# Performance work log

Hardware: AMD Instinct MI355X
Metric: run time of the kernel (lower is better)

## Reference

```python
import jax, jax.numpy as jnp
import numpy as np

B, L, DM, H = 2, 2048, 512, 8
D = DM // H
FACTOR = 5
NUM_K = int(FACTOR * np.ceil(np.log(L)))  # 40
NUM_Q = NUM_K  # q_len == k_len here
EPS = 1e-5


def setup_inputs() -> dict:
    key = jax.random.key(0)
    ks = jax.random.split(key, 12)
    s = DM ** -0.5
    return {
        "q": jax.random.normal(ks[0], (B, L, DM), jnp.float32),
        "k": jax.random.normal(ks[1], (B, L, DM), jnp.float32),
        "v": jax.random.normal(ks[2], (B, L, DM), jnp.float32),
        "Wq": jax.random.normal(ks[3], (DM, DM), jnp.float32) * s,
        "bq": jnp.zeros((DM,), jnp.float32),
        "Wk": jax.random.normal(ks[4], (DM, DM), jnp.float32) * s,
        "bk": jnp.zeros((DM,), jnp.float32),
        "Wv": jax.random.normal(ks[5], (DM, DM), jnp.float32) * s,
        "bv": jnp.zeros((DM,), jnp.float32),
        "gamma": jnp.ones((DM,), jnp.float32),
        "beta": jnp.zeros((DM,), jnp.float32),
        "random_index": jax.random.randint(ks[6], (L, NUM_K), 0, L, jnp.int32),
    }


def _heads(x):
    # [B, L, DM] -> [B, H, L, D]
    return x.reshape(B, L, H, D).transpose(0, 2, 1, 3)


def reference(q, k, v, Wq, bq, Wk, bk, Wv, bv, gamma, beta, random_index):
    qp = _heads(q @ Wq + bq)
    kp = _heads(k @ Wk + bk)
    vp = _heads(v @ Wv + bv)

    # ProbSparse: sample NUM_K keys per query position (shared over batch/head)
    k_samp = kp[:, :, random_index, :]                      # [B,H,L,NUM_K,D]
    pre = jnp.einsum('bhid,bhijd->bhij', qp, k_samp)        # [B,H,L,NUM_K]
    measure = pre.max(-1) - pre.sum(-1) / L                 # sparsity measure [B,H,L]
    _, q_idx = jax.lax.top_k(measure, NUM_Q)                # [B,H,NUM_Q]

    q_sel = jnp.take_along_axis(qp, q_idx[..., None], axis=2)   # [B,H,NUM_Q,D]
    attn = jnp.einsum('bhid,bhjd->bhij', q_sel, kp) * D ** -0.5 # [B,H,NUM_Q,L]
    attn = jax.nn.softmax(attn, axis=-1)                    # dropout = identity (eval)
    out_sel = jnp.einsum('bhij,bhjd->bhid', attn, vp)       # [B,H,NUM_Q,D]

    # use_mask=False path: context is the mean of v over keys
    v_mean = vp.mean(axis=2)                                # [B,H,D]
    context = jnp.broadcast_to(v_mean[:, :, None, :], (B, H, L, D))
    bi = jnp.arange(B)[:, None, None]
    hi = jnp.arange(H)[None, :, None]
    out = context.at[bi, hi, q_idx].set(out_sel)            # scatter selected rows

    out = out.transpose(0, 2, 1, 3).reshape(B, L, DM)
    y = out + q
    mu = y.mean(-1, keepdims=True)
    var = y.var(-1, keepdims=True)
    yn = (y - mu) / jnp.sqrt(var + EPS) * gamma + beta
    return (yn, attn)
```

## Files before the change

### kernel.cpp

```cpp
#include <hip/hip_runtime.h>
#include <math.h>

#define BB 2
#define LL 2048
#define DMM 512
#define HH 8
#define DD 64
#define NUMK 40
#define NUMQ 40
#define LNEPS 1e-5f
#define LSEG 128
#define NLS 16

typedef unsigned short ushort_t;
typedef __attribute__((ext_vector_type(8))) short bf16x8;
typedef __attribute__((ext_vector_type(4))) float f32x4;

__device__ inline ushort_t f2bf(float x) {
    union { float f; unsigned int u; } v; v.f = x;
    unsigned int r = v.u + 0x7fffu + ((v.u >> 16) & 1u);
    return (ushort_t)(r >> 16);
}
__device__ inline float bf2f(ushort_t h) {
    union { unsigned int u; float f; } v; v.u = ((unsigned int)h) << 16;
    return v.f;
}

__global__ __launch_bounds__(256) void convert_x_kernel(
    const float* __restrict__ q, const float* __restrict__ k, const float* __restrict__ v,
    ushort_t* __restrict__ Xh, ushort_t* __restrict__ Xl) {
    const size_t plane = (size_t)BB * LL * DMM;
    const float* X = (blockIdx.y == 0) ? q : (blockIdx.y == 1) ? k : v;
    ushort_t* xh = Xh + plane * blockIdx.y;
    ushort_t* xl = Xl + plane * blockIdx.y;
    const size_t base = ((size_t)blockIdx.x * 256 + threadIdx.x) * 8;
    float4 a = *(const float4*)(X + base);
    float4 b = *(const float4*)(X + base + 4);
    float xs[8] = {a.x, a.y, a.z, a.w, b.x, b.y, b.z, b.w};
    unsigned int hp[4], lp[4];
#pragma unroll
    for (int j = 0; j < 4; ++j) {
        ushort_t h0 = f2bf(xs[2 * j]),     h1 = f2bf(xs[2 * j + 1]);
        ushort_t l0 = f2bf(xs[2 * j] - bf2f(h0));
        ushort_t l1 = f2bf(xs[2 * j + 1] - bf2f(h1));
        hp[j] = (unsigned int)h0 | ((unsigned int)h1 << 16);
        lp[j] = (unsigned int)l0 | ((unsigned int)l1 << 16);
    }
    *(uint4*)(xh + base) = make_uint4(hp[0], hp[1], hp[2], hp[3]);
    *(uint4*)(xl + base) = make_uint4(lp[0], lp[1], lp[2], lp[3]);
}

__global__ __launch_bounds__(256) void convert_w_kernel(
    const float* __restrict__ Wq, const float* __restrict__ Wk, const float* __restrict__ Wv,
    ushort_t* __restrict__ Wht, ushort_t* __restrict__ Wlt) {
    __shared__ float tile[64][65];
    const size_t plane = (size_t)DMM * DMM;
    const float* W = (blockIdx.z == 0) ? Wq : (blockIdx.z == 1) ? Wk : Wv;
    ushort_t* wht = Wht + plane * blockIdx.z;
    ushort_t* wlt = Wlt + plane * blockIdx.z;
    const int n0 = blockIdx.x * 64, k0 = blockIdx.y * 64;
    const int t = threadIdx.x;
    const int d = t & 63, g = t >> 6;
    for (int rr = g; rr < 64; rr += 4)
        tile[rr][d] = W[(size_t)(k0 + rr) * DMM + n0 + d];
    __syncthreads();
    for (int cc = g; cc < 64; cc += 4) {
        float x = tile[d][cc];
        ushort_t hi = f2bf(x);
        ushort_t lo = f2bf(x - bf2f(hi));
        wht[(size_t)(n0 + cc) * DMM + k0 + d] = hi;
        wlt[(size_t)(n0 + cc) * DMM + k0 + d] = lo;
    }
}

__device__ inline void stage_one(const ushort_t* __restrict__ g, ushort_t* lbuf,
                                 int r0, int lane, int k0) {
    const int r = r0 + (lane >> 3);
    const int c = (lane & 7) ^ (r & 7);
    const ushort_t* gp = g + (size_t)r * DMM + k0 + c * 8;
    __builtin_amdgcn_global_load_lds(
        (const __attribute__((address_space(1))) unsigned int*)gp,
        (__attribute__((address_space(3))) unsigned int*)(lbuf + (size_t)r0 * 64),
        16, 0, 0);
}
__device__ inline bf16x8 frag_ld(const ushort_t* buf, int row, int c) {
    const int idx = row * 8 + (c ^ (row & 7));
    return *(const bf16x8*)(buf + idx * 8);
}

__global__ __launch_bounds__(256, 2) void proj_mfma_kernel(
    const ushort_t* __restrict__ Xh, const ushort_t* __restrict__ Xl,
    const ushort_t* __restrict__ Wht, const ushort_t* __restrict__ Wlt,
    const float* __restrict__ bq, const float* __restrict__ bk, const float* __restrict__ bv,
    float* __restrict__ Oq, float* __restrict__ Ok, float* __restrict__ Ov) {
    const int orig = blockIdx.x;
    const int c = (orig & 7) * 48 + (orig >> 3);
    const int jb = c & 3, mb = (c >> 2) & 31, z = c >> 7;

    const size_t xplane = (size_t)BB * LL * DMM;
    const size_t wplane = (size_t)DMM * DMM;
    const ushort_t* ah_g = Xh + xplane * z;
    const ushort_t* al_g = Xl + xplane * z;
    const ushort_t* bh_g = Wht + wplane * z;
    const ushort_t* bl_g = Wlt + wplane * z;
    const float* bias = (z == 0) ? bq : (z == 1) ? bk : bv;
    float* Out = (z == 0) ? Oq : (z == 1) ? Ok : Ov;

    __shared__ __align__(16) ushort_t bufAh[128 * 64];
    __shared__ __align__(16) ushort_t bufAl[128 * 64];
    __shared__ __align__(16) ushort_t bufBh[128 * 64];
    __shared__ __align__(16) ushort_t bufBl[128 * 64];

    const int t = threadIdx.x;
    const int lane = t & 63, w = t >> 6;
    const int wm = (w & 1) * 64, wn = (w >> 1) * 64;
    const int m0 = mb * 128, j0 = jb * 128;

    const ushort_t* A_h = ah_g + (size_t)m0 * DMM;
    const ushort_t* A_l = al_g + (size_t)m0 * DMM;
    const ushort_t* B_h = bh_g + (size_t)j0 * DMM;
    const ushort_t* B_l = bl_g + (size_t)j0 * DMM;

    f32x4 acc[4][4];
#pragma unroll
    for (int i = 0; i < 4; ++i)
#pragma unroll
        for (int j = 0; j < 4; ++j) acc[i][j] = (f32x4){0.f, 0.f, 0.f, 0.f};

    for (int ch = 0; ch < 8; ++ch) {
        const int k0 = ch * 64;
#pragma unroll
        for (int i = 0; i < 4; ++i) {
            const int r0 = (w * 4 + i) * 8;
            stage_one(A_h, bufAh, r0, lane, k0);
            stage_one(A_l, bufAl, r0, lane, k0);
            stage_one(B_h, bufBh, r0, lane, k0);
            stage_one(B_l, bufBl, r0, lane, k0);
        }
        __syncthreads();
#pragma unroll
        for (int ks = 0; ks < 2; ++ks) {
            const int cc = ks * 4 + (lane >> 4);
            bf16x8 fah[4], fal[4];
#pragma unroll
            for (int tm = 0; tm < 4; ++tm) {
                const int row = wm + tm * 16 + (lane & 15);
                fah[tm] = frag_ld(bufAh, row, cc);
                fal[tm] = frag_ld(bufAl, row, cc);
            }
#pragma unroll
            for (int tn = 0; tn < 4; ++tn) {
                const int rowb = wn + tn * 16 + (lane & 15);
                const bf16x8 fbh = frag_ld(bufBh, rowb, cc);
                const bf16x8 fbl = frag_ld(bufBl, rowb, cc);
#pragma unroll
                for (int tm = 0; tm < 4; ++tm) {
                    acc[tm][tn] = __builtin_amdgcn_mfma_f32_16x16x32_bf16(fah[tm], fbh, acc[tm][tn], 0, 0, 0);
                    acc[tm][tn] = __builtin_amdgcn_mfma_f32_16x16x32_bf16(fal[tm], fbh, acc[tm][tn], 0, 0, 0);
                    acc[tm][tn] = __builtin_amdgcn_mfma_f32_16x16x32_bf16(fah[tm], fbl, acc[tm][tn], 0, 0, 0);
                }
            }
        }
        __syncthreads();
    }

#pragma unroll
    for (int tn = 0; tn < 4; ++tn) {
        const int gn = j0 + wn + tn * 16 + (lane & 15);
        const float bvv = bias[gn];
        const int h = gn >> 6, d = gn & 63;
#pragma unroll
        for (int tm = 0; tm < 4; ++tm) {
#pragma unroll
            for (int reg = 0; reg < 4; ++reg) {
                const int gm = m0 + wm + tm * 16 + (lane >> 4) * 4 + reg;
                const int b = gm >> 11, l = gm & (LL - 1);
                Out[(((size_t)(b * HH + h)) * LL + l) * DD + d] = acc[tm][tn][reg] + bvv;
            }
        }
    }
}

__global__ __launch_bounds__(256) void measure_kernel(const float* __restrict__ qp2,
                                                      const float* __restrict__ kp2,
                                                      const int* __restrict__ rnd,
                                                      float* __restrict__ measure) {
    const int t = threadIdx.x;
    const int lane = t & 63;
    const int wv = t >> 6;
    const int g = lane >> 4;
    const int dq = (lane & 15) * 4;
    const int bh = blockIdx.x;
    const int i = blockIdx.y * 16 + wv * 4 + g;
    const float4 qv = *(const float4*)(qp2 + ((size_t)bh * LL + i) * DD + dq);
    const float* kbase = kp2 + (size_t)bh * LL * DD;
    const int* rp = rnd + i * NUMK;
    float mx = -INFINITY, sm = 0.f;
#pragma unroll 8
    for (int j = 0; j < NUMK; ++j) {
        const int row = rp[j];
        const float4 kv = *(const float4*)(kbase + (size_t)row * DD + dq);
        float p = kv.x * qv.x;
        p = fmaf(kv.y, qv.y, p); p = fmaf(kv.z, qv.z, p); p = fmaf(kv.w, qv.w, p);
        p += __shfl_xor(p, 1, 64);
        p += __shfl_xor(p, 2, 64);
        p += __shfl_xor(p, 4, 64);
        p += __shfl_xor(p, 8, 64);
        mx = fmaxf(mx, p);
        sm += p;
    }
    if ((lane & 15) == 0) measure[(size_t)bh * LL + i] = mx - sm * (1.0f / LL);
}

__global__ __launch_bounds__(256) void topk_kernel(const float* __restrict__ measure,
                                                   int* __restrict__ q_idx,
                                                   int* __restrict__ sel_pos) {
    __shared__ unsigned int keys[LL];
    __shared__ int hist[256];
    __shared__ unsigned int prefix_sh;
    __shared__ int need_sh;
    __shared__ unsigned int cval[256];
    __shared__ int cidx[256];
    __shared__ int cnt;
    const int t = threadIdx.x;
    const int bh = blockIdx.x;
    for (int i = t; i < LL; i += 256) {
        const float f = measure[(size_t)bh * LL + i];
        unsigned int u = __float_as_uint(f);
        keys[i] = (u & 0x80000000u) ? ~u : (u | 0x80000000u);
        sel_pos[(size_t)bh * LL + i] = -1;
    }
    if (t == 0) { prefix_sh = 0u; need_sh = NUMQ; cnt = 0; }
    __syncthreads();

    for (int round = 0; round < 4; ++round) {
        const int shift = 24 - round * 8;
        hist[t] = 0;
        __syncthreads();
        const unsigned int pref = prefix_sh;
        const unsigned int mask = (round == 0) ? 0u : (0xFFFFFFFFu << (shift + 8));
        for (int i = t; i < LL; i += 256) {
            const unsigned int key = keys[i];
            if ((key & mask) == pref)
                atomicAdd(&hist[(key >> shift) & 0xFF], 1);
        }
        __syncthreads();
        if (t == 0) {
            const int need = need_sh;
            int acc = 0;
            int v = 255;
            for (; v > 0; --v) {
                if (acc + hist[v] >= need) break;
                acc += hist[v];
            }
            need_sh = need - acc;
            prefix_sh = pref | ((unsigned int)v << shift);
        }
        __syncthreads();
    }
    const unsigned int K40 = prefix_sh;

    for (int i = t; i < LL; i += 256) {
        if (keys[i] >= K40) {
            int p = atomicAdd(&cnt, 1);
            if (p < 256) { cval[p] = keys[i]; cidx[p] = i; }
        }
    }
    __syncthreads();
    int M = cnt; if (M > 256) M = 256;
    for (int i = t; i < M; i += 256) {
        const unsigned int ki = cval[i];
        const int ii = cidx[i];
        int r = 0;
        for (int j = 0; j < M; ++j) {
            const unsigned int kj = cval[j];
            r += (kj > ki || (kj == ki && cidx[j] < ii)) ? 1 : 0;
        }
        if (r < NUMQ) {
            q_idx[bh * NUMQ + r] = ii;
            sel_pos[(size_t)bh * LL + ii] = r;
        }
    }
}

__global__ __launch_bounds__(256) void attn_part_kernel(
    const float* __restrict__ qp2, const float* __restrict__ kp2,
    const float* __restrict__ vp2, const int* __restrict__ q_idx,
    float* __restrict__ attn_out, float* __restrict__ part_m,
    float* __restrict__ part_s, float* __restrict__ part_pv) {
    __shared__ __align__(16) float Qs[NUMQ][68];
    __shared__ __align__(16) float Ks[LSEG * 64];
    __shared__ __align__(16) float Vs[LSEG * 64];
    __shared__ __align__(16) float Ss[NUMQ][136];
    const int t = threadIdx.x;
    const int lane = t & 63, w = t >> 6;
    const int bh = blockIdx.x;
    const int ls = blockIdx.y;
    const int l0 = ls * LSEG;

    for (int idx = t; idx < NUMQ * 16; idx += 256) {
        const int r = idx >> 4, c4 = idx & 15;
        const int qi = q_idx[bh * NUMQ + r];
        float4 v = *(const float4*)(qp2 + ((size_t)bh * LL + qi) * DD + c4 * 4);
        Qs[r][c4 * 4 + 0] = v.x * 0.125f;
        Qs[r][c4 * 4 + 1] = v.y * 0.125f;
        Qs[r][c4 * 4 + 2] = v.z * 0.125f;
        Qs[r][c4 * 4 + 3] = v.w * 0.125f;
    }

    const float* kseg = kp2 + ((size_t)bh * LL + l0) * DD;
    const float* vseg = vp2 + ((size_t)bh * LL + l0) * DD;
#pragma unroll
    for (int i = 0; i < 8; ++i) {
        const int r0 = (w * 8 + i) * 4;
        const int r = r0 + (lane >> 4);
        const int cg = (lane & 15) ^ (r & 15);
        __builtin_amdgcn_global_load_lds(
            (const __attribute__((address_space(1))) unsigned int*)(kseg + (size_t)r * DD + cg * 4),
            (__attribute__((address_space(3))) unsigned int*)(Ks + r0 * 64), 16, 0, 0);
        __builtin_amdgcn_global_load_lds(
            (const __attribute__((address_space(1))) unsigned int*)(vseg + (size_t)r * DD + cg * 4),
            (__attribute__((address_space(3))) unsigned int*)(Vs + r0 * 64), 16, 0, 0);
    }
    __syncthreads();

    const int qt = t >> 5;
    const int jt = t & 31;
    float acc[5][4];
#pragma unroll
    for (int i = 0; i < 5; ++i)
#pragma unroll
        for (int jj = 0; jj < 4; ++jj) acc[i][jj] = 0.f;

    for (int c4 = 0; c4 < 16; ++c4) {
        float4 q4[5];
#pragma unroll
        for (int i = 0; i < 5; ++i)
            q4[i] = *(const float4*)&Qs[qt + 8 * i][c4 * 4];
#pragma unroll
        for (int jj = 0; jj < 4; ++jj) {
            const int r = jt + 32 * jj;
            const float4 k4 = *(const float4*)&Ks[r * 64 + ((c4 ^ (r & 15)) * 4)];
#pragma unroll
            for (int i = 0; i < 5; ++i) {
                acc[i][jj] = fmaf(q4[i].x, k4.x, acc[i][jj]);
                acc[i][jj] = fmaf(q4[i].y, k4.y, acc[i][jj]);
                acc[i][jj] = fmaf(q4[i].z, k4.z, acc[i][jj]);
                acc[i][jj] = fmaf(q4[i].w, k4.w, acc[i][jj]);
            }
        }
    }

#pragma unroll
    for (int i = 0; i < 5; ++i) {
        const int r = qt + 8 * i;
        float m = fmaxf(fmaxf(acc[i][0], acc[i][1]), fmaxf(acc[i][2], acc[i][3]));
        m = fmaxf(m, __shfl_xor(m, 16, 64));
        m = fmaxf(m, __shfl_xor(m, 8, 64));
        m = fmaxf(m, __shfl_xor(m, 4, 64));
        m = fmaxf(m, __shfl_xor(m, 2, 64));
        m = fmaxf(m, __shfl_xor(m, 1, 64));
        float p0 = __expf(acc[i][0] - m), p1 = __expf(acc[i][1] - m);
        float p2 = __expf(acc[i][2] - m), p3 = __expf(acc[i][3] - m);
        Ss[r][jt]      = p0;
        Ss[r][jt + 32] = p1;
        Ss[r][jt + 64] = p2;
        Ss[r][jt + 96] = p3;
        float s = p0 + p1 + p2 + p3;
        s += __shfl_xor(s, 16, 64);
        s += __shfl_xor(s, 8, 64);
        s += __shfl_xor(s, 4, 64);
        s += __shfl_xor(s, 2, 64);
        s += __shfl_xor(s, 1, 64);
        if (jt == 0) {
            const int row = bh * NUMQ + r;
            part_m[row * NLS + ls] = m;
            part_s[row * NLS + ls] = s;
        }
    }
    __syncthreads();

    for (int idx = t; idx < NUMQ * 32; idx += 256) {
        const int r = idx >> 5, c4 = idx & 31;
        const float4 v = *(const float4*)&Ss[r][c4 * 4];
        *(float4*)(attn_out + (size_t)(bh * NUMQ + r) * LL + l0 + c4 * 4) = v;
    }

    const int dt = t & 31;
    float o[5][2];
#pragma unroll
    for (int i = 0; i < 5; ++i) { o[i][0] = 0.f; o[i][1] = 0.f; }
#pragma unroll 4
    for (int j = 0; j < LSEG; ++j) {
        const int pg = (dt >> 1) ^ (j & 15);
        const float* vr = &Vs[j * 64 + pg * 4 + (dt & 1) * 2];
        const float v0 = vr[0], v1 = vr[1];
#pragma unroll
        for (int i = 0; i < 5; ++i) {
            const float p = Ss[qt + 8 * i][j];
            o[i][0] = fmaf(p, v0, o[i][0]);
            o[i][1] = fmaf(p, v1, o[i][1]);
        }
    }
#pragma unroll
    for (int i = 0; i < 5; ++i) {
        const int row = bh * NUMQ + qt + 8 * i;
        float* pp = part_pv + ((size_t)row * NLS + ls) * DD + dt * 2;
        pp[0] = o[i][0];
        pp[1] = o[i][1];
    }
}

__global__ __launch_bounds__(256) void attn_fin_kernel(
    const float* __restrict__ part_m, const float* __restrict__ part_s,
    const float* __restrict__ part_pv, float* __restrict__ attn_out,
    float* __restrict__ out_sel) {
    const int row = blockIdx.x;
    const int t = threadIdx.x;
    float M = -INFINITY;
#pragma unroll
    for (int i = 0; i < NLS; ++i) M = fmaxf(M, part_m[row * NLS + i]);
    float T = 0.f;
#pragma unroll
    for (int i = 0; i < NLS; ++i)
        T += part_s[row * NLS + i] * __expf(part_m[row * NLS + i] - M);
    const float inv = 1.0f / T;
    float* arow = attn_out + (size_t)row * LL;
    {
        const int s0 = t >> 5;
        const float g0 = __expf(part_m[row * NLS + s0] - M) * inv;
        const float g1 = __expf(part_m[row * NLS + 8 + s0] - M) * inv;
        float4 v0 = *(const float4*)&arow[4 * t];
        float4 v1 = *(const float4*)&arow[1024 + 4 * t];
        v0.x *= g0; v0.y *= g0; v0.z *= g0; v0.w *= g0;
        v1.x *= g1; v1.y *= g1; v1.z *= g1; v1.w *= g1;
        *(float4*)&arow[4 * t] = v0;
        *(float4*)&arow[1024 + 4 * t] = v1;
    }
    if (t < DD) {
        float s = 0.f;
#pragma unroll
        for (int i = 0; i < NLS; ++i)
            s += part_pv[((size_t)row * NLS + i) * DD + t] * __expf(part_m[row * NLS + i] - M);
        out_sel[(size_t)row * DD + t] = s * inv;
    }
}

__global__ __launch_bounds__(256) void vmean1_kernel(const float* __restrict__ vp2,
                                                     float* __restrict__ partial) {
    __shared__ float pv[256];
    const int t = threadIdx.x;
    const int chunk = blockIdx.x & 31;
    const int bh = blockIdx.x >> 5;
    const int d = t & 63, g = t >> 6;
    const int l0 = chunk * 64;
    float acc = 0.f;
    for (int l = l0 + g; l < l0 + 64; l += 4)
        acc += vp2[((size_t)bh * LL + l) * DD + d];
    pv[t] = acc;
    __syncthreads();
    if (t < 64)
        partial[(size_t)blockIdx.x * 64 + t] = pv[t] + pv[64 + t] + pv[128 + t] + pv[192 + t];
}

__global__ __launch_bounds__(64) void vmean2_kernel(const float* __restrict__ partial,
                                                    float* __restrict__ v_mean) {
    const int bh = blockIdx.x;
    const int t = threadIdx.x;
    float s = 0.f;
    for (int c = 0; c < 32; ++c)
        s += partial[((size_t)bh * 32 + c) * 64 + t];
    v_mean[bh * 64 + t] = s * (1.0f / LL);
}

__global__ __launch_bounds__(512) void final_kernel(const float* __restrict__ q_in,
                                                    const int* __restrict__ sel_pos,
                                                    const float* __restrict__ out_sel,
                                                    const float* __restrict__ v_mean,
                                                    const float* __restrict__ gamma,
                                                    const float* __restrict__ beta,
                                                    float* __restrict__ yout) {
    __shared__ float wred[8];
    const int j = threadIdx.x;
    const int lane = j & 63, wv = j >> 6;
    const int tok = blockIdx.x;
    const int b = tok >> 11;
    const int l = tok & (LL - 1);
    const int h = wv, d = lane;
    const int bh = b * HH + h;
    const int p = sel_pos[(size_t)bh * LL + l];
    float val = (p >= 0) ? out_sel[((size_t)bh * NUMQ + p) * DD + d]
                         : v_mean[bh * DD + d];
    float y = val + q_in[(size_t)tok * DMM + j];
    float s = y;
#pragma unroll
    for (int off = 32; off > 0; off >>= 1) s += __shfl_xor(s, off, 64);
    if (lane == 0) wred[wv] = s;
    __syncthreads();
    float tot = 0.f;
#pragma unroll
    for (int u = 0; u < 8; ++u) tot += wred[u];
    float mu = tot * (1.0f / DMM);
    __syncthreads();
    float dv = y - mu;
    float s2 = dv * dv;
#pragma unroll
    for (int off = 32; off > 0; off >>= 1) s2 += __shfl_xor(s2, off, 64);
    if (lane == 0) wred[wv] = s2;
    __syncthreads();
    float tot2 = 0.f;
#pragma unroll
    for (int u = 0; u < 8; ++u) tot2 += wred[u];
    float var = tot2 * (1.0f / DMM);
    float yn = dv * rsqrtf(var + LNEPS) * gamma[j] + beta[j];
    yout[(size_t)tok * DMM + j] = yn;
}

extern "C" void kernel_launch(void* const* d_in, const int* in_sizes, int n_in,
                              void* d_out, int out_size, void* d_ws, size_t ws_size,
                              hipStream_t stream) {
    const float* q     = (const float*)d_in[0];
    const float* k     = (const float*)d_in[1];
    const float* v     = (const float*)d_in[2];
    const float* Wq    = (const float*)d_in[3];
    const float* bq    = (const float*)d_in[4];
    const float* Wk    = (const float*)d_in[5];
    const float* bk    = (const float*)d_in[6];
    const float* Wv    = (const float*)d_in[7];
    const float* bv    = (const float*)d_in[8];
    const float* gamma = (const float*)d_in[9];
    const float* beta  = (const float*)d_in[10];
    const int*   rnd   = (const int*)d_in[11];

    float* ws = (float*)d_ws;
    const size_t proj_sz = (size_t)BB * HH * LL * DD;
    float* qp2     = ws;
    float* kp2     = qp2 + proj_sz;
    float* vp2     = kp2 + proj_sz;
    float* measure = vp2 + proj_sz;
    float* out_sel = measure + (size_t)BB * HH * LL;
    float* v_mean  = out_sel + (size_t)BB * HH * NUMQ * DD;
    float* partial = v_mean + (size_t)BB * HH * DD;
    float* part_m  = partial + (size_t)BB * HH * 32 * 64;
    float* part_s  = part_m + (size_t)BB * HH * NUMQ * NLS;
    float* part_pv = part_s + (size_t)BB * HH * NUMQ * NLS;
    int*   q_idx   = (int*)(part_pv + (size_t)BB * HH * NUMQ * NLS * DD);
    int*   sel_pos = q_idx + BB * HH * NUMQ;
    ushort_t* Xh  = (ushort_t*)(sel_pos + BB * HH * LL);
    ushort_t* Xl  = Xh + 3 * proj_sz;
    ushort_t* Wht = Xl + 3 * proj_sz;
    ushort_t* Wlt = Wht + 3 * (size_t)DMM * DMM;

    float* yn_out   = (float*)d_out;
    float* attn_out = yn_out + (size_t)BB * LL * DMM;

    convert_x_kernel<<<dim3(BB * LL * DMM / (256 * 8), 3), 256, 0, stream>>>(q, k, v, Xh, Xl);
    convert_w_kernel<<<dim3(DMM / 64, DMM / 64, 3), 256, 0, stream>>>(Wq, Wk, Wv, Wht, Wlt);
    proj_mfma_kernel<<<dim3(3 * (BB * LL / 128) * (DMM / 128), 1, 1), 256, 0, stream>>>(
        Xh, Xl, Wht, Wlt, bq, bk, bv, qp2, kp2, vp2);
    vmean1_kernel<<<BB * HH * 32, 256, 0, stream>>>(vp2, partial);
    vmean2_kernel<<<BB * HH, 64, 0, stream>>>(partial, v_mean);
    measure_kernel<<<dim3(BB * HH, LL / 16), 256, 0, stream>>>(qp2, kp2, rnd, measure);
    topk_kernel<<<BB * HH, 256, 0, stream>>>(measure, q_idx, sel_pos);
    attn_part_kernel<<<dim3(BB * HH, NLS), 256, 0, stream>>>(
        qp2, kp2, vp2, q_idx, attn_out, part_m, part_s, part_pv);
    attn_fin_kernel<<<BB * HH * NUMQ, 256, 0, stream>>>(
        part_m, part_s, part_pv, attn_out, out_sel);
    final_kernel<<<BB * LL, 512, 0, stream>>>(q, sel_pos, out_sel, v_mean, gamma, beta, yn_out);
}
```

Before: 213.8 us.

## Merge small kernels to cut launch count and fold attention finalization into LayerNorm

Merges the two conversion kernels into one launch and fuses the v-mean partial sum into the measure kernel. The v-mean reduction moves into the top-k kernel, and attention finalization merges into the final LayerNorm kernel, which recomputes the selected output rows from the partial softmax stats. This takes the launch count from nine to five to cut launch overhead and small-kernel tails. It also vectorizes the P·V inner loop with float4 loads of the score rows. The cost is that the selected-row rescale is recomputed per token and lanes in the fused kernels diverge.

```diff
diff --git a/kernel.cpp b/kernel.cpp
--- a/kernel.cpp
+++ b/kernel.cpp
@@ -26,50 +26,54 @@
     return v.f;
 }
 
-__global__ __launch_bounds__(256) void convert_x_kernel(
+__global__ __launch_bounds__(256) void convert_all_kernel(
     const float* __restrict__ q, const float* __restrict__ k, const float* __restrict__ v,
-    ushort_t* __restrict__ Xh, ushort_t* __restrict__ Xl) {
-    const size_t plane = (size_t)BB * LL * DMM;
-    const float* X = (blockIdx.y == 0) ? q : (blockIdx.y == 1) ? k : v;
-    ushort_t* xh = Xh + plane * blockIdx.y;
-    ushort_t* xl = Xl + plane * blockIdx.y;
-    const size_t base = ((size_t)blockIdx.x * 256 + threadIdx.x) * 8;
-    float4 a = *(const float4*)(X + base);
-    float4 b = *(const float4*)(X + base + 4);
-    float xs[8] = {a.x, a.y, a.z, a.w, b.x, b.y, b.z, b.w};
-    unsigned int hp[4], lp[4];
-#pragma unroll
-    for (int j = 0; j < 4; ++j) {
-        ushort_t h0 = f2bf(xs[2 * j]),     h1 = f2bf(xs[2 * j + 1]);
-        ushort_t l0 = f2bf(xs[2 * j] - bf2f(h0));
-        ushort_t l1 = f2bf(xs[2 * j + 1] - bf2f(h1));
-        hp[j] = (unsigned int)h0 | ((unsigned int)h1 << 16);
-        lp[j] = (unsigned int)l0 | ((unsigned int)l1 << 16);
-    }
-    *(uint4*)(xh + base) = make_uint4(hp[0], hp[1], hp[2], hp[3]);
-    *(uint4*)(xl + base) = make_uint4(lp[0], lp[1], lp[2], lp[3]);
-}
-
-__global__ __launch_bounds__(256) void convert_w_kernel(
     const float* __restrict__ Wq, const float* __restrict__ Wk, const float* __restrict__ Wv,
+    ushort_t* __restrict__ Xh, ushort_t* __restrict__ Xl,
     ushort_t* __restrict__ Wht, ushort_t* __restrict__ Wlt) {
     __shared__ float tile[64][65];
-    const size_t plane = (size_t)DMM * DMM;
-    const float* W = (blockIdx.z == 0) ? Wq : (blockIdx.z == 1) ? Wk : Wv;
-    ushort_t* wht = Wht + plane * blockIdx.z;
-    ushort_t* wlt = Wlt + plane * blockIdx.z;
-    const int n0 = blockIdx.x * 64, k0 = blockIdx.y * 64;
+    const int bx = blockIdx.x;
     const int t = threadIdx.x;
-    const int d = t & 63, g = t >> 6;
-    for (int rr = g; rr < 64; rr += 4)
-        tile[rr][d] = W[(size_t)(k0 + rr) * DMM + n0 + d];
-    __syncthreads();
-    for (int cc = g; cc < 64; cc += 4) {
-        float x = tile[d][cc];
-        ushort_t hi = f2bf(x);
-        ushort_t lo = f2bf(x - bf2f(hi));
-        wht[(size_t)(n0 + cc) * DMM + k0 + d] = hi;
-        wlt[(size_t)(n0 + cc) * DMM + k0 + d] = lo;
+    if (bx < 3072) {
+        const int y = bx >> 10, x = bx & 1023;
+        const size_t plane = (size_t)BB * LL * DMM;
+        const float* X = (y == 0) ? q : (y == 1) ? k : v;
+        ushort_t* xh = Xh + plane * y;
+        ushort_t* xl = Xl + plane * y;
+        const size_t base = ((size_t)x * 256 + t) * 8;
+        float4 a = *(const float4*)(X + base);
+        float4 b = *(const float4*)(X + base + 4);
+        float xs[8] = {a.x, a.y, a.z, a.w, b.x, b.y, b.z, b.w};
+        unsigned int hp[4], lp[4];
+#pragma unroll
+        for (int j = 0; j < 4; ++j) {
+            ushort_t h0 = f2bf(xs[2 * j]),     h1 = f2bf(xs[2 * j + 1]);
+            ushort_t l0 = f2bf(xs[2 * j] - bf2f(h0));
+            ushort_t l1 = f2bf(xs[2 * j + 1] - bf2f(h1));
+            hp[j] = (unsigned int)h0 | ((unsigned int)h1 << 16);
+            lp[j] = (unsigned int)l0 | ((unsigned int)l1 << 16);
+        }
+        *(uint4*)(xh + base) = make_uint4(hp[0], hp[1], hp[2], hp[3]);
+        *(uint4*)(xl + base) = make_uint4(lp[0], lp[1], lp[2], lp[3]);
+    } else {
+        const int idx = bx - 3072;
+        const int z = idx >> 6, rem = idx & 63;
+        const size_t plane = (size_t)DMM * DMM;
+        const float* W = (z == 0) ? Wq : (z == 1) ? Wk : Wv;
+        ushort_t* wht = Wht + plane * z;
+        ushort_t* wlt = Wlt + plane * z;
+        const int n0 = (rem & 7) * 64, k0 = (rem >> 3) * 64;
+        const int d = t & 63, g = t >> 6;
+        for (int rr = g; rr < 64; rr += 4)
+            tile[rr][d] = W[(size_t)(k0 + rr) * DMM + n0 + d];
+        __syncthreads();
+        for (int cc = g; cc < 64; cc += 4) {
+            float x = tile[d][cc];
+            ushort_t hi = f2bf(x);
+            ushort_t lo = f2bf(x - bf2f(hi));
+            wht[(size_t)(n0 + cc) * DMM + k0 + d] = hi;
+            wlt[(size_t)(n0 + cc) * DMM + k0 + d] = lo;
+        }
     }
 }
 
@@ -181,40 +185,59 @@
     }
 }
 
-__global__ __launch_bounds__(256) void measure_kernel(const float* __restrict__ qp2,
-                                                      const float* __restrict__ kp2,
-                                                      const int* __restrict__ rnd,
-                                                      float* __restrict__ measure) {
+__global__ __launch_bounds__(256) void measure_vmean_kernel(
+    const float* __restrict__ qp2, const float* __restrict__ kp2,
+    const float* __restrict__ vp2, const int* __restrict__ rnd,
+    float* __restrict__ measure, float* __restrict__ partial) {
+    __shared__ float pv[256];
+    const int bx = blockIdx.x;
     const int t = threadIdx.x;
-    const int lane = t & 63;
-    const int wv = t >> 6;
-    const int g = lane >> 4;
-    const int dq = (lane & 15) * 4;
-    const int bh = blockIdx.x;
-    const int i = blockIdx.y * 16 + wv * 4 + g;
-    const float4 qv = *(const float4*)(qp2 + ((size_t)bh * LL + i) * DD + dq);
-    const float* kbase = kp2 + (size_t)bh * LL * DD;
-    const int* rp = rnd + i * NUMK;
-    float mx = -INFINITY, sm = 0.f;
+    if (bx < 2048) {
+        const int lane = t & 63;
+        const int wv = t >> 6;
+        const int g = lane >> 4;
+        const int dq = (lane & 15) * 4;
+        const int bh = bx >> 7;
+        const int i = (bx & 127) * 16 + wv * 4 + g;
+        const float4 qv = *(const float4*)(qp2 + ((size_t)bh * LL + i) * DD + dq);
+        const float* kbase = kp2 + (size_t)bh * LL * DD;
+        const int* rp = rnd + i * NUMK;
+        float mx = -INFINITY, sm = 0.f;
 #pragma unroll 8
-    for (int j = 0; j < NUMK; ++j) {
-        const int row = rp[j];
-        const float4 kv = *(const float4*)(kbase + (size_t)row * DD + dq);
-        float p = kv.x * qv.x;
-        p = fmaf(kv.y, qv.y, p); p = fmaf(kv.z, qv.z, p); p = fmaf(kv.w, qv.w, p);
-        p += __shfl_xor(p, 1, 64);
-        p += __shfl_xor(p, 2, 64);
-        p += __shfl_xor(p, 4, 64);
-        p += __shfl_xor(p, 8, 64);
-        mx = fmaxf(mx, p);
-        sm += p;
-    }
-    if ((lane & 15) == 0) measure[(size_t)bh * LL + i] = mx - sm * (1.0f / LL);
+        for (int j = 0; j < NUMK; ++j) {
+            const int row = rp[j];
+            const float4 kv = *(const float4*)(kbase + (size_t)row * DD + dq);
+            float p = kv.x * qv.x;
+            p = fmaf(kv.y, qv.y, p); p = fmaf(kv.z, qv.z, p); p = fmaf(kv.w, qv.w, p);
+            p += __shfl_xor(p, 1, 64);
+            p += __shfl_xor(p, 2, 64);
+            p += __shfl_xor(p, 4, 64);
+            p += __shfl_xor(p, 8, 64);
+            mx = fmaxf(mx, p);
+            sm += p;
+        }
+        if ((lane & 15) == 0) measure[(size_t)bh * LL + i] = mx - sm * (1.0f / LL);
+    } else {
+        const int idx = bx - 2048;
+        const int chunk = idx & 31;
+        const int bh = idx >> 5;
+        const int d = t & 63, g = t >> 6;
+        const int l0 = chunk * 64;
+        float acc = 0.f;
+        for (int l = l0 + g; l < l0 + 64; l += 4)
+            acc += vp2[((size_t)bh * LL + l) * DD + d];
+        pv[t] = acc;
+        __syncthreads();
+        if (t < 64)
+            partial[(size_t)idx * 64 + t] = pv[t] + pv[64 + t] + pv[128 + t] + pv[192 + t];
+    }
 }
 
 __global__ __launch_bounds__(256) void topk_kernel(const float* __restrict__ measure,
+                                                   const float* __restrict__ partial,
                                                    int* __restrict__ q_idx,
-                                                   int* __restrict__ sel_pos) {
+                                                   int* __restrict__ sel_pos,
+                                                   float* __restrict__ v_mean) {
     __shared__ unsigned int keys[LL];
     __shared__ int hist[256];
     __shared__ unsigned int prefix_sh;
@@ -229,6 +252,12 @@
         unsigned int u = __float_as_uint(f);
         keys[i] = (u & 0x80000000u) ? ~u : (u | 0x80000000u);
         sel_pos[(size_t)bh * LL + i] = -1;
+    }
+    if (t < 64) {
+        float s = 0.f;
+        for (int c = 0; c < 32; ++c)
+            s += partial[((size_t)bh * 32 + c) * 64 + t];
+        v_mean[bh * 64 + t] = s * (1.0f / LL);
     }
     if (t == 0) { prefix_sh = 0u; need_sh = NUMQ; cnt = 0; }
     __syncthreads();
@@ -390,16 +419,24 @@
     float o[5][2];
 #pragma unroll
     for (int i = 0; i < 5; ++i) { o[i][0] = 0.f; o[i][1] = 0.f; }
-#pragma unroll 4
-    for (int j = 0; j < LSEG; ++j) {
-        const int pg = (dt >> 1) ^ (j & 15);
-        const float* vr = &Vs[j * 64 + pg * 4 + (dt & 1) * 2];
-        const float v0 = vr[0], v1 = vr[1];
-#pragma unroll
-        for (int i = 0; i < 5; ++i) {
-            const float p = Ss[qt + 8 * i][j];
-            o[i][0] = fmaf(p, v0, o[i][0]);
-            o[i][1] = fmaf(p, v1, o[i][1]);
+#pragma unroll 2
+    for (int j0_ = 0; j0_ < LSEG; j0_ += 4) {
+        float4 p4[5];
+#pragma unroll
+        for (int i = 0; i < 5; ++i)
+            p4[i] = *(const float4*)&Ss[qt + 8 * i][j0_];
+#pragma unroll
+        for (int jj = 0; jj < 4; ++jj) {
+            const int j = j0_ + jj;
+            const int pg = (dt >> 1) ^ (j & 15);
+            const float* vr = &Vs[j * 64 + pg * 4 + (dt & 1) * 2];
+            const float v0 = vr[0], v1 = vr[1];
+#pragma unroll
+            for (int i = 0; i < 5; ++i) {
+                const float p = ((const float*)&p4[i])[jj];
+                o[i][0] = fmaf(p, v0, o[i][0]);
+                o[i][1] = fmaf(p, v1, o[i][1]);
+            }
         }
     }
 #pragma unroll
@@ -411,86 +448,57 @@
     }
 }
 
-__global__ __launch_bounds__(256) void attn_fin_kernel(
+__global__ __launch_bounds__(512) void final_all_kernel(
+    const float* __restrict__ q_in, const int* __restrict__ sel_pos,
     const float* __restrict__ part_m, const float* __restrict__ part_s,
-    const float* __restrict__ part_pv, float* __restrict__ attn_out,
-    float* __restrict__ out_sel) {
-    const int row = blockIdx.x;
-    const int t = threadIdx.x;
-    float M = -INFINITY;
-#pragma unroll
-    for (int i = 0; i < NLS; ++i) M = fmaxf(M, part_m[row * NLS + i]);
-    float T = 0.f;
-#pragma unroll
-    for (int i = 0; i < NLS; ++i)
-        T += part_s[row * NLS + i] * __expf(part_m[row * NLS + i] - M);
-    const float inv = 1.0f / T;
-    float* arow = attn_out + (size_t)row * LL;
-    {
-        const int s0 = t >> 5;
-        const float g0 = __expf(part_m[row * NLS + s0] - M) * inv;
-        const float g1 = __expf(part_m[row * NLS + 8 + s0] - M) * inv;
-        float4 v0 = *(const float4*)&arow[4 * t];
-        float4 v1 = *(const float4*)&arow[1024 + 4 * t];
-        v0.x *= g0; v0.y *= g0; v0.z *= g0; v0.w *= g0;
-        v1.x *= g1; v1.y *= g1; v1.z *= g1; v1.w *= g1;
-        *(float4*)&arow[4 * t] = v0;
-        *(float4*)&arow[1024 + 4 * t] = v1;
-    }
-    if (t < DD) {
-        float s = 0.f;
+    const float* __restrict__ part_pv, const float* __restrict__ v_mean,
+    const float* __restrict__ gamma, const float* __restrict__ beta,
+    float* __restrict__ attn_out, float* __restrict__ yout) {
+    __shared__ float wred[8];
+    const int bx = blockIdx.x;
+    const int j = threadIdx.x;
+    if (bx >= BB * LL) {
+        const int row = bx - BB * LL;
+        float M = -INFINITY;
+#pragma unroll
+        for (int i = 0; i < NLS; ++i) M = fmaxf(M, part_m[row * NLS + i]);
+        float T = 0.f;
 #pragma unroll
         for (int i = 0; i < NLS; ++i)
-            s += part_pv[((size_t)row * NLS + i) * DD + t] * __expf(part_m[row * NLS + i] - M);
-        out_sel[(size_t)row * DD + t] = s * inv;
-    }
-}
-
-__global__ __launch_bounds__(256) void vmean1_kernel(const float* __restrict__ vp2,
-                                                     float* __restrict__ partial) {
-    __shared__ float pv[256];
-    const int t = threadIdx.x;
-    const int chunk = blockIdx.x & 31;
-    const int bh = blockIdx.x >> 5;
-    const int d = t & 63, g = t >> 6;
-    const int l0 = chunk * 64;
-    float acc = 0.f;
-    for (int l = l0 + g; l < l0 + 64; l += 4)
-        acc += vp2[((size_t)bh * LL + l) * DD + d];
-    pv[t] = acc;
-    __syncthreads();
-    if (t < 64)
-        partial[(size_t)blockIdx.x * 64 + t] = pv[t] + pv[64 + t] + pv[128 + t] + pv[192 + t];
-}
-
-__global__ __launch_bounds__(64) void vmean2_kernel(const float* __restrict__ partial,
-                                                    float* __restrict__ v_mean) {
-    const int bh = blockIdx.x;
-    const int t = threadIdx.x;
-    float s = 0.f;
-    for (int c = 0; c < 32; ++c)
-        s += partial[((size_t)bh * 32 + c) * 64 + t];
-    v_mean[bh * 64 + t] = s * (1.0f / LL);
-}
-
-__global__ __launch_bounds__(512) void final_kernel(const float* __restrict__ q_in,
-                                                    const int* __restrict__ sel_pos,
-                                                    const float* __restrict__ out_sel,
-                                                    const float* __restrict__ v_mean,
-                                                    const float* __restrict__ gamma,
-                                                    const float* __restrict__ beta,
-                                                    float* __restrict__ yout) {
-    __shared__ float wred[8];
-    const int j = threadIdx.x;
+            T += part_s[row * NLS + i] * __expf(part_m[row * NLS + i] - M);
+        const float inv = 1.0f / T;
+        const int s0 = j >> 5;
+        const float g = __expf(part_m[row * NLS + s0] - M) * inv;
+        float* arow = attn_out + (size_t)row * LL;
+        float4 v = *(const float4*)&arow[4 * j];
+        v.x *= g; v.y *= g; v.z *= g; v.w *= g;
+        *(float4*)&arow[4 * j] = v;
+        return;
+    }
     const int lane = j & 63, wv = j >> 6;
-    const int tok = blockIdx.x;
+    const int tok = bx;
     const int b = tok >> 11;
     const int l = tok & (LL - 1);
     const int h = wv, d = lane;
     const int bh = b * HH + h;
     const int p = sel_pos[(size_t)bh * LL + l];
-    float val = (p >= 0) ? out_sel[((size_t)bh * NUMQ + p) * DD + d]
-                         : v_mean[bh * DD + d];
+    float val;
+    if (p >= 0) {
+        const int row = bh * NUMQ + p;
+        float M = -INFINITY;
+#pragma unroll
+        for (int i = 0; i < NLS; ++i) M = fmaxf(M, part_m[row * NLS + i]);
+        float T = 0.f, s = 0.f;
+#pragma unroll
+        for (int i = 0; i < NLS; ++i) {
+            const float e = __expf(part_m[row * NLS + i] - M);
+            T += part_s[row * NLS + i] * e;
+            s += part_pv[((size_t)row * NLS + i) * DD + d] * e;
+        }
+        val = s * (1.0f / T);
+    } else {
+        val = v_mean[bh * DD + d];
+    }
     float y = val + q_in[(size_t)tok * DMM + j];
     float s = y;
 #pragma unroll
@@ -554,17 +562,13 @@
     float* yn_out   = (float*)d_out;
     float* attn_out = yn_out + (size_t)BB * LL * DMM;
 
-    convert_x_kernel<<<dim3(BB * LL * DMM / (256 * 8), 3), 256, 0, stream>>>(q, k, v, Xh, Xl);
-    convert_w_kernel<<<dim3(DMM / 64, DMM / 64, 3), 256, 0, stream>>>(Wq, Wk, Wv, Wht, Wlt);
+    convert_all_kernel<<<3072 + 192, 256, 0, stream>>>(q, k, v, Wq, Wk, Wv, Xh, Xl, Wht, Wlt);
     proj_mfma_kernel<<<dim3(3 * (BB * LL / 128) * (DMM / 128), 1, 1), 256, 0, stream>>>(
         Xh, Xl, Wht, Wlt, bq, bk, bv, qp2, kp2, vp2);
-    vmean1_kernel<<<BB * HH * 32, 256, 0, stream>>>(vp2, partial);
-    vmean2_kernel<<<BB * HH, 64, 0, stream>>>(partial, v_mean);
-    measure_kernel<<<dim3(BB * HH, LL / 16), 256, 0, stream>>>(qp2, kp2, rnd, measure);
-    topk_kernel<<<BB * HH, 256, 0, stream>>>(measure, q_idx, sel_pos);
+    measure_vmean_kernel<<<2048 + 512, 256, 0, stream>>>(qp2, kp2, vp2, rnd, measure, partial);
+    topk_kernel<<<BB * HH, 256, 0, stream>>>(measure, partial, q_idx, sel_pos, v_mean);
     attn_part_kernel<<<dim3(BB * HH, NLS), 256, 0, stream>>>(
         qp2, kp2, vp2, q_idx, attn_out, part_m, part_s, part_pv);
-    attn_fin_kernel<<<BB * HH * NUMQ, 256, 0, stream>>>(
-        part_m, part_s, part_pv, attn_out, out_sel);
-    final_kernel<<<BB * LL, 512, 0, stream>>>(q, sel_pos, out_sel, v_mean, gamma, beta, yn_out);
-}
+    final_all_kernel<<<BB * LL + BB * HH * NUMQ, 512, 0, stream>>>(
+        q, sel_pos, part_m, part_s, part_pv, v_mean, gamma, beta, attn_out, yn_out);
+}
```

Result: faster. 205.0 us (-4.1%).
